# Performance work log

Measured on AMD Instinct MI355X. Metric: run time of the kernel, lower is better.

## Reference

```python
import jax, jax.numpy as jnp
import numpy as np

B, YS, XS, H = 16, 256, 256, 128  # batch, image height (y_size), width (x_size), MLP hidden


def setup_inputs() -> dict:
    key = jax.random.key(0)
    ks = jax.random.split(key, 6)
    images = jax.random.normal(ks[0], (B, YS, XS), dtype=jnp.float32)

    def glorot(k, shape):
        fan_in = shape[0]
        return (jax.random.normal(k, shape, dtype=jnp.float32) / np.float32(np.sqrt(fan_in)))

    W1 = glorot(ks[1], (3, H));  b1 = jnp.zeros((H,), jnp.float32)
    W2 = glorot(ks[2], (H, H));  b2 = jnp.zeros((H,), jnp.float32)
    W3 = glorot(ks[3], (H, H));  b3 = jnp.zeros((H,), jnp.float32)
    W4 = glorot(ks[4], (H, 1));  b4 = jnp.zeros((1,), jnp.float32)
    return {
        "images": images,
        "W1": W1, "b1": b1, "W2": W2, "b2": b2,
        "W3": W3, "b3": b3, "W4": W4, "b4": b4,
        "diffusion_weight": jnp.float32(0.1),
        "n": 0,
    }


def reference(images, W1, b1, W2, b2, W3, b3, W4, b4, diffusion_weight, n):
    # NOTE: in the original torch module, diffusion_loss (and all autograd
    # derivatives) are computed but never added to total_loss; only
    # boundary_loss accumulates. We reproduce exactly that math.
    Bn, y_size, x_size = images.shape
    x = jnp.linspace(-x_size / 2, x_size / 2, x_size, dtype=images.dtype)
    y = jnp.linspace(-y_size / 2, y_size / 2, y_size, dtype=images.dtype)
    Xg, Yg = jnp.meshgrid(x, y, indexing="ij")  # (x_size, y_size), x-major
    xf = Xg.ravel()  # (N,) with N = x_size*y_size
    yf = Yg.ravel()

    # t_recon is all-zeros in the original, so T_recon_i = i + n*B (constant field).
    ts = jnp.arange(Bn, dtype=images.dtype) + jnp.asarray(n * Bn, images.dtype)  # (B,)

    def field(tval):
        tf = jnp.zeros_like(xf) + tval
        inp = jnp.stack([xf, yf, tf], axis=-1)          # (N, 3)
        h = jnp.tanh(inp @ W1 + b1)
        h = jnp.tanh(h @ W2 + b2)
        h = jnp.tanh(h @ W3 + b3)
        return (h @ W4 + b4)[:, 0]                       # (N,)

    surface_recon = jax.vmap(field)(ts)                  # (B, N)
    # matches torch: surface_recon.view(y_size, x_size) on the ij-flattened field
    recon = surface_recon.reshape(Bn, y_size, x_size)
    boundary = jnp.mean((images - recon) ** 2, axis=(1, 2))  # per-sample
    return jnp.sum(boundary) / Bn
```

## Files before the change

kernel.cpp:

```cpp
#include <hip/hip_runtime.h>
#include <hip/hip_bf16.h>


#define BATCH 16
#define LDA 136
#define STEP (256.0f / 255.0f)
#define KS 2.8853900817779268f

typedef __bf16 v8bf __attribute__((ext_vector_type(8)));
typedef float  v4f  __attribute__((ext_vector_type(4)));

__device__ __forceinline__ unsigned short f2bf(float f) {
    unsigned int u = __float_as_uint(f);
    unsigned int r = (u + 0x7fffu + ((u >> 16) & 1u)) >> 16;
    return (unsigned short)r;
}

#if __has_builtin(__builtin_amdgcn_perm)
__device__ __forceinline__ unsigned int pack2bf(float a, float b) {
    return __builtin_amdgcn_perm(__float_as_uint(b), __float_as_uint(a), 0x07060302u);
}
#else
__device__ __forceinline__ unsigned int pack2bf(float a, float b) {
    return (__float_as_uint(a) >> 16) | (__float_as_uint(b) & 0xffff0000u);
}
#endif

__device__ __forceinline__ float tanh_pre(float zk) {
    float e = __builtin_amdgcn_exp2f(zk);
    float r = __builtin_amdgcn_rcpf(e + 1.f);
    return fmaf(-2.f, r, 1.f);
}

__global__ __launch_bounds__(256) void prep_kernel(
    const float* __restrict__ W2, const float* __restrict__ W3,
    unsigned short* __restrict__ w2t, unsigned short* __restrict__ w3t,
    float* __restrict__ partials, unsigned int* __restrict__ counter)
{
    int o = blockIdx.x * 256 + threadIdx.x;
    if (o < 1024) partials[o] = 0.f;
    if (o == 0) *counter = 0u;
    const float* src = (o < 16384) ? W2 : W3;
    unsigned short* dst = (o < 16384) ? w2t : w3t;
    int e = o & 16383;
    int k = e >> 7, n = e & 127;
    dst[n * 128 + k] = f2bf(src[e] * KS);
}

__global__ __launch_bounds__(512, 8) void main_kernel(
    const float* __restrict__ images,
    const float* __restrict__ W1, const float* __restrict__ b1,
    const float* __restrict__ b2, const float* __restrict__ b3,
    const float* __restrict__ W4, const float* __restrict__ b4,
    const int*   __restrict__ np,
    const unsigned short* __restrict__ w2t,
    const unsigned short* __restrict__ w3t,
    float* __restrict__ partials, unsigned int* __restrict__ counter,
    float* __restrict__ out)
{
    __shared__ unsigned short A[128 * LDA];
    __shared__ float P[8][128];
    __shared__ float red[8];
    __shared__ unsigned int isLastS;

    const int tid  = threadIdx.x;
    const int lane = tid & 63;
    const int w    = tid >> 6;
    const int l15  = lane & 15;
    const int quad = lane >> 4;

    const int bid = blockIdx.x;
    const int b   = bid >> 9;
    const int rem = bid & 511;
    const int r   = rem >> 1;
    const int c0  = (rem & 1) << 7;

    const float tv = (float)(b + np[0] * BATCH);
    const float xv = -128.f + (float)r * STEP;

    {
        const int lo = tid & 31, hi = tid >> 5;
        const int j0 = lo * 4, p0 = hi * 8;
        float4 wx = *(const float4*)(W1 + j0);
        float4 wy = *(const float4*)(W1 + 128 + j0);
        float4 wt = *(const float4*)(W1 + 256 + j0);
        float4 bb = *(const float4*)(b1 + j0);
        float wy0 = KS * wy.x, wy1 = KS * wy.y, wy2 = KS * wy.z, wy3 = KS * wy.w;
        const float yv0 = fmaf((float)(c0 + p0), STEP, -128.f);
        float z0 = fmaf(yv0, wy0, KS * fmaf(xv, wx.x, fmaf(tv, wt.x, bb.x)));
        float z1 = fmaf(yv0, wy1, KS * fmaf(xv, wx.y, fmaf(tv, wt.y, bb.y)));
        float z2 = fmaf(yv0, wy2, KS * fmaf(xv, wx.z, fmaf(tv, wt.z, bb.z)));
        float z3 = fmaf(yv0, wy3, KS * fmaf(xv, wx.w, fmaf(tv, wt.w, bb.w)));
        const float d0 = STEP * wy0, d1 = STEP * wy1, d2 = STEP * wy2, d3 = STEP * wy3;
        #pragma unroll
        for (int pi = 0; pi < 8; ++pi) {
            uint2 u = make_uint2(pack2bf(tanh_pre(z0), tanh_pre(z1)),
                                 pack2bf(tanh_pre(z2), tanh_pre(z3)));
            *(uint2*)&A[(p0 + pi) * LDA + j0] = u;
            z0 += d0; z1 += d1; z2 += d2; z3 += d3;
        }
    }
    __syncthreads();

    const int colw = w * 16 + l15;
    const int ch4  = w * 16 + quad * 4;

    v8bf wf[4];
    #pragma unroll
    for (int ks = 0; ks < 4; ++ks)
        wf[ks] = *(const v8bf*)(w2t + colw * 128 + ks * 32 + quad * 8);

    v4f acc[8];
    {
        float4 b2q = *(const float4*)(b2 + ch4);
        v4f ini = (v4f){b2q.x * KS, b2q.y * KS, b2q.z * KS, b2q.w * KS};
        #pragma unroll
        for (int mt = 0; mt < 8; ++mt) acc[mt] = ini;
    }
    #pragma unroll
    for (int ks = 0; ks < 4; ++ks) {
        #pragma unroll
        for (int mt = 0; mt < 8; ++mt) {
            v8bf af = *(const v8bf*)&A[(mt * 16 + l15) * LDA + ks * 32 + quad * 8];
            acc[mt] = __builtin_amdgcn_mfma_f32_16x16x32_bf16(wf[ks], af, acc[mt], 0, 0, 0);
        }
    }

    v8bf w3f[4];
    #pragma unroll
    for (int ks = 0; ks < 4; ++ks)
        w3f[ks] = *(const v8bf*)(w3t + colw * 128 + ks * 32 + quad * 8);
    __syncthreads();

    #pragma unroll
    for (int mt = 0; mt < 8; ++mt) {
        uint2 u = make_uint2(pack2bf(tanh_pre(acc[mt][0]), tanh_pre(acc[mt][1])),
                             pack2bf(tanh_pre(acc[mt][2]), tanh_pre(acc[mt][3])));
        *(uint2*)&A[(mt * 16 + l15) * LDA + ch4] = u;
    }
    __syncthreads();

    {
        float4 b3q = *(const float4*)(b3 + ch4);
        v4f ini = (v4f){b3q.x * KS, b3q.y * KS, b3q.z * KS, b3q.w * KS};
        #pragma unroll
        for (int mt = 0; mt < 8; ++mt) acc[mt] = ini;
    }
    #pragma unroll
    for (int ks = 0; ks < 4; ++ks) {
        #pragma unroll
        for (int mt = 0; mt < 8; ++mt) {
            v8bf af = *(const v8bf*)&A[(mt * 16 + l15) * LDA + ks * 32 + quad * 8];
            acc[mt] = __builtin_amdgcn_mfma_f32_16x16x32_bf16(w3f[ks], af, acc[mt], 0, 0, 0);
        }
    }

    {
        float4 w4q = *(const float4*)(W4 + ch4);
        #pragma unroll
        for (int mt = 0; mt < 8; ++mt) {
            float s;
            s  = tanh_pre(acc[mt][0]) * w4q.x;
            s  = fmaf(tanh_pre(acc[mt][1]), w4q.y, s);
            s  = fmaf(tanh_pre(acc[mt][2]), w4q.z, s);
            s  = fmaf(tanh_pre(acc[mt][3]), w4q.w, s);
            s += __shfl_xor(s, 16, 64);
            s += __shfl_xor(s, 32, 64);
            if (quad == 0) P[w][mt * 16 + l15] = s;
        }
    }
    __syncthreads();

    {
        float e2 = 0.f;
        if (tid < 128) {
            float s = b4[0];
            #pragma unroll
            for (int ww = 0; ww < 8; ++ww) s += P[ww][tid];
            float img = images[(b << 16) + (r << 8) + c0 + tid];
            float err = img - s;
            e2 = err * err;
        }
        #pragma unroll
        for (int off = 1; off < 64; off <<= 1)
            e2 += __shfl_xor(e2, off, 64);
        if (lane == 0 && tid < 128)
            atomicAdd(&partials[bid & 1023], e2);
    }

    __syncthreads();
    if (tid == 0)
        isLastS = (atomicAdd(counter, 1u) == (unsigned)(gridDim.x - 1)) ? 1u : 0u;
    __syncthreads();
    if (isLastS) {
        float s = __hip_atomic_load(&partials[tid],       __ATOMIC_RELAXED, __HIP_MEMORY_SCOPE_AGENT)
                + __hip_atomic_load(&partials[tid + 512], __ATOMIC_RELAXED, __HIP_MEMORY_SCOPE_AGENT);
        #pragma unroll
        for (int off = 1; off < 64; off <<= 1)
            s += __shfl_xor(s, off, 64);
        if (lane == 0) red[w] = s;
        __syncthreads();
        if (tid == 0) {
            float tot = 0.f;
            #pragma unroll
            for (int i = 0; i < 8; ++i) tot += red[i];
            out[0] = tot * (1.f / 1048576.f);
        }
    }
}

extern "C" void kernel_launch(void* const* d_in, const int* in_sizes, int n_in,
                              void* d_out, int out_size, void* d_ws, size_t ws_size,
                              hipStream_t stream)
{
    const float* images = (const float*)d_in[0];
    const float* W1 = (const float*)d_in[1];
    const float* b1 = (const float*)d_in[2];
    const float* W2 = (const float*)d_in[3];
    const float* b2 = (const float*)d_in[4];
    const float* W3 = (const float*)d_in[5];
    const float* b3 = (const float*)d_in[6];
    const float* W4 = (const float*)d_in[7];
    const float* b4 = (const float*)d_in[8];
    const int*   np = (const int*)d_in[10];

    unsigned short* w2t = (unsigned short*)d_ws;
    unsigned short* w3t = w2t + 128 * 128;
    float* partials = (float*)((char*)d_ws + 65536);
    unsigned int* counter = (unsigned int*)((char*)d_ws + 65536 + 4096);

    prep_kernel<<<128, 256, 0, stream>>>(W2, W3, w2t, w3t, partials, counter);
    main_kernel<<<BATCH * 256 * 2, 512, 0, stream>>>(
        images, W1, b1, b2, b3, W4, b4, np, w2t, w3t, partials, counter, (float*)d_out);
}
```

Before: 192.6 us.

## Retile MLP MFMA work to 32 cols x 64 rows per wave; exp-recurrence for layer1 tanh

Each wave now covers 32 output channels over half of the 128 pixels, so every A fragment read from LDS feeds two MFMAs and total LDS fragment reads drop. Weight fragments are loaded from global per k-step instead of being held in registers up front. The first-layer tanh replaces the additive z recurrence with a multiplicative exp recurrence, one exp2 per step turned into one multiply. The exp recurrence can accumulate rounding error or overflow for large weights, and the partial-sum buffer shrinks to four rows.

```diff
diff --git a/kernel.cpp b/kernel.cpp
--- a/kernel.cpp
+++ b/kernel.cpp
@@ -59,7 +59,7 @@
     float* __restrict__ out)
 {
     __shared__ unsigned short A[128 * LDA];
-    __shared__ float P[8][128];
+    __shared__ float P[4][128];
     __shared__ float red[8];
     __shared__ unsigned int isLastS;
 
@@ -85,88 +85,107 @@
         float4 wy = *(const float4*)(W1 + 128 + j0);
         float4 wt = *(const float4*)(W1 + 256 + j0);
         float4 bb = *(const float4*)(b1 + j0);
-        float wy0 = KS * wy.x, wy1 = KS * wy.y, wy2 = KS * wy.z, wy3 = KS * wy.w;
         const float yv0 = fmaf((float)(c0 + p0), STEP, -128.f);
-        float z0 = fmaf(yv0, wy0, KS * fmaf(xv, wx.x, fmaf(tv, wt.x, bb.x)));
-        float z1 = fmaf(yv0, wy1, KS * fmaf(xv, wx.y, fmaf(tv, wt.y, bb.y)));
-        float z2 = fmaf(yv0, wy2, KS * fmaf(xv, wx.z, fmaf(tv, wt.z, bb.z)));
-        float z3 = fmaf(yv0, wy3, KS * fmaf(xv, wx.w, fmaf(tv, wt.w, bb.w)));
-        const float d0 = STEP * wy0, d1 = STEP * wy1, d2 = STEP * wy2, d3 = STEP * wy3;
+        float z0 = fmaf(yv0, KS * wy.x, KS * fmaf(xv, wx.x, fmaf(tv, wt.x, bb.x)));
+        float z1 = fmaf(yv0, KS * wy.y, KS * fmaf(xv, wx.y, fmaf(tv, wt.y, bb.y)));
+        float z2 = fmaf(yv0, KS * wy.z, KS * fmaf(xv, wx.z, fmaf(tv, wt.z, bb.z)));
+        float z3 = fmaf(yv0, KS * wy.w, KS * fmaf(xv, wx.w, fmaf(tv, wt.w, bb.w)));
+        float e0 = __builtin_amdgcn_exp2f(z0);
+        float e1 = __builtin_amdgcn_exp2f(z1);
+        float e2 = __builtin_amdgcn_exp2f(z2);
+        float e3 = __builtin_amdgcn_exp2f(z3);
+        const float E0 = __builtin_amdgcn_exp2f(KS * STEP * wy.x);
+        const float E1 = __builtin_amdgcn_exp2f(KS * STEP * wy.y);
+        const float E2 = __builtin_amdgcn_exp2f(KS * STEP * wy.z);
+        const float E3 = __builtin_amdgcn_exp2f(KS * STEP * wy.w);
         #pragma unroll
         for (int pi = 0; pi < 8; ++pi) {
-            uint2 u = make_uint2(pack2bf(tanh_pre(z0), tanh_pre(z1)),
-                                 pack2bf(tanh_pre(z2), tanh_pre(z3)));
+            float h0 = fmaf(-2.f, __builtin_amdgcn_rcpf(e0 + 1.f), 1.f);
+            float h1 = fmaf(-2.f, __builtin_amdgcn_rcpf(e1 + 1.f), 1.f);
+            float h2 = fmaf(-2.f, __builtin_amdgcn_rcpf(e2 + 1.f), 1.f);
+            float h3 = fmaf(-2.f, __builtin_amdgcn_rcpf(e3 + 1.f), 1.f);
+            uint2 u = make_uint2(pack2bf(h0, h1), pack2bf(h2, h3));
             *(uint2*)&A[(p0 + pi) * LDA + j0] = u;
-            z0 += d0; z1 += d1; z2 += d2; z3 += d3;
-        }
-    }
-    __syncthreads();
-
-    const int colw = w * 16 + l15;
-    const int ch4  = w * 16 + quad * 4;
-
-    v8bf wf[4];
-    #pragma unroll
-    for (int ks = 0; ks < 4; ++ks)
-        wf[ks] = *(const v8bf*)(w2t + colw * 128 + ks * 32 + quad * 8);
-
-    v4f acc[8];
-    {
-        float4 b2q = *(const float4*)(b2 + ch4);
-        v4f ini = (v4f){b2q.x * KS, b2q.y * KS, b2q.z * KS, b2q.w * KS};
-        #pragma unroll
-        for (int mt = 0; mt < 8; ++mt) acc[mt] = ini;
+            e0 *= E0; e1 *= E1; e2 *= E2; e3 *= E3;
+        }
+    }
+    __syncthreads();
+
+    const int cg   = w & 3;
+    const int ph   = w >> 2;
+    const int colw = cg * 32 + l15;
+    const int ch4  = cg * 32 + quad * 4;
+
+    v4f acc[2][4];
+    {
+        float4 ba = *(const float4*)(b2 + ch4);
+        float4 bc = *(const float4*)(b2 + ch4 + 16);
+        v4f ia = (v4f){ba.x * KS, ba.y * KS, ba.z * KS, ba.w * KS};
+        v4f ic = (v4f){bc.x * KS, bc.y * KS, bc.z * KS, bc.w * KS};
+        #pragma unroll
+        for (int mt = 0; mt < 4; ++mt) { acc[0][mt] = ia; acc[1][mt] = ic; }
     }
     #pragma unroll
     for (int ks = 0; ks < 4; ++ks) {
-        #pragma unroll
-        for (int mt = 0; mt < 8; ++mt) {
-            v8bf af = *(const v8bf*)&A[(mt * 16 + l15) * LDA + ks * 32 + quad * 8];
-            acc[mt] = __builtin_amdgcn_mfma_f32_16x16x32_bf16(wf[ks], af, acc[mt], 0, 0, 0);
-        }
-    }
-
-    v8bf w3f[4];
+        v8bf wa = *(const v8bf*)(w2t + colw * 128 + ks * 32 + quad * 8);
+        v8bf wb = *(const v8bf*)(w2t + (colw + 16) * 128 + ks * 32 + quad * 8);
+        #pragma unroll
+        for (int mt = 0; mt < 4; ++mt) {
+            v8bf af = *(const v8bf*)&A[(ph * 64 + mt * 16 + l15) * LDA + ks * 32 + quad * 8];
+            acc[0][mt] = __builtin_amdgcn_mfma_f32_16x16x32_bf16(wa, af, acc[0][mt], 0, 0, 0);
+            acc[1][mt] = __builtin_amdgcn_mfma_f32_16x16x32_bf16(wb, af, acc[1][mt], 0, 0, 0);
+        }
+    }
+    __syncthreads();
+
     #pragma unroll
-    for (int ks = 0; ks < 4; ++ks)
-        w3f[ks] = *(const v8bf*)(w3t + colw * 128 + ks * 32 + quad * 8);
-    __syncthreads();
-
-    #pragma unroll
-    for (int mt = 0; mt < 8; ++mt) {
-        uint2 u = make_uint2(pack2bf(tanh_pre(acc[mt][0]), tanh_pre(acc[mt][1])),
-                             pack2bf(tanh_pre(acc[mt][2]), tanh_pre(acc[mt][3])));
-        *(uint2*)&A[(mt * 16 + l15) * LDA + ch4] = u;
-    }
-    __syncthreads();
-
-    {
-        float4 b3q = *(const float4*)(b3 + ch4);
-        v4f ini = (v4f){b3q.x * KS, b3q.y * KS, b3q.z * KS, b3q.w * KS};
-        #pragma unroll
-        for (int mt = 0; mt < 8; ++mt) acc[mt] = ini;
+    for (int ct = 0; ct < 2; ++ct) {
+        #pragma unroll
+        for (int mt = 0; mt < 4; ++mt) {
+            uint2 u = make_uint2(pack2bf(tanh_pre(acc[ct][mt][0]), tanh_pre(acc[ct][mt][1])),
+                                 pack2bf(tanh_pre(acc[ct][mt][2]), tanh_pre(acc[ct][mt][3])));
+            *(uint2*)&A[(ph * 64 + mt * 16 + l15) * LDA + ch4 + ct * 16] = u;
+        }
+    }
+    __syncthreads();
+
+    {
+        float4 ba = *(const float4*)(b3 + ch4);
+        float4 bc = *(const float4*)(b3 + ch4 + 16);
+        v4f ia = (v4f){ba.x * KS, ba.y * KS, ba.z * KS, ba.w * KS};
+        v4f ic = (v4f){bc.x * KS, bc.y * KS, bc.z * KS, bc.w * KS};
+        #pragma unroll
+        for (int mt = 0; mt < 4; ++mt) { acc[0][mt] = ia; acc[1][mt] = ic; }
     }
     #pragma unroll
     for (int ks = 0; ks < 4; ++ks) {
-        #pragma unroll
-        for (int mt = 0; mt < 8; ++mt) {
-            v8bf af = *(const v8bf*)&A[(mt * 16 + l15) * LDA + ks * 32 + quad * 8];
-            acc[mt] = __builtin_amdgcn_mfma_f32_16x16x32_bf16(w3f[ks], af, acc[mt], 0, 0, 0);
-        }
-    }
-
-    {
-        float4 w4q = *(const float4*)(W4 + ch4);
-        #pragma unroll
-        for (int mt = 0; mt < 8; ++mt) {
+        v8bf wa = *(const v8bf*)(w3t + colw * 128 + ks * 32 + quad * 8);
+        v8bf wb = *(const v8bf*)(w3t + (colw + 16) * 128 + ks * 32 + quad * 8);
+        #pragma unroll
+        for (int mt = 0; mt < 4; ++mt) {
+            v8bf af = *(const v8bf*)&A[(ph * 64 + mt * 16 + l15) * LDA + ks * 32 + quad * 8];
+            acc[0][mt] = __builtin_amdgcn_mfma_f32_16x16x32_bf16(wa, af, acc[0][mt], 0, 0, 0);
+            acc[1][mt] = __builtin_amdgcn_mfma_f32_16x16x32_bf16(wb, af, acc[1][mt], 0, 0, 0);
+        }
+    }
+
+    {
+        float4 w4a = *(const float4*)(W4 + ch4);
+        float4 w4b = *(const float4*)(W4 + ch4 + 16);
+        #pragma unroll
+        for (int mt = 0; mt < 4; ++mt) {
             float s;
-            s  = tanh_pre(acc[mt][0]) * w4q.x;
-            s  = fmaf(tanh_pre(acc[mt][1]), w4q.y, s);
-            s  = fmaf(tanh_pre(acc[mt][2]), w4q.z, s);
-            s  = fmaf(tanh_pre(acc[mt][3]), w4q.w, s);
+            s = tanh_pre(acc[0][mt][0]) * w4a.x;
+            s = fmaf(tanh_pre(acc[0][mt][1]), w4a.y, s);
+            s = fmaf(tanh_pre(acc[0][mt][2]), w4a.z, s);
+            s = fmaf(tanh_pre(acc[0][mt][3]), w4a.w, s);
+            s = fmaf(tanh_pre(acc[1][mt][0]), w4b.x, s);
+            s = fmaf(tanh_pre(acc[1][mt][1]), w4b.y, s);
+            s = fmaf(tanh_pre(acc[1][mt][2]), w4b.z, s);
+            s = fmaf(tanh_pre(acc[1][mt][3]), w4b.w, s);
             s += __shfl_xor(s, 16, 64);
             s += __shfl_xor(s, 32, 64);
-            if (quad == 0) P[w][mt * 16 + l15] = s;
+            if (quad == 0) P[cg][ph * 64 + mt * 16 + l15] = s;
         }
     }
     __syncthreads();
@@ -174,9 +193,7 @@
     {
         float e2 = 0.f;
         if (tid < 128) {
-            float s = b4[0];
-            #pragma unroll
-            for (int ww = 0; ww < 8; ++ww) s += P[ww][tid];
+            float s = b4[0] + P[0][tid] + P[1][tid] + P[2][tid] + P[3][tid];
             float img = images[(b << 16) + (r << 8) + c0 + tid];
             float err = img - s;
             e2 = err * err;
```

After: 234.1 us. 21.6% more time.
